# Optimization experiments

Hardware: AMD Instinct MI355X
Metric: run time of the kernel (lower is better)

The kernel has to match this reference:

```python
import jax, jax.numpy as jnp
import numpy as np

D_MODEL = 1024
N_HEADS = 16
DEPTH = D_MODEL // N_HEADS  # 64
BATCH, SEQ = 4, 2048


def setup_inputs() -> dict:
    key = jax.random.key(0)
    ks = jax.random.split(key, 8)
    x = jax.random.normal(ks[0], (BATCH, SEQ, D_MODEL), dtype=jnp.float32)
    # Per-head Dense(depth) weights stacked over heads: [H, d_model, depth]
    s = 1.0 / np.sqrt(D_MODEL)
    Wq = jax.random.normal(ks[1], (N_HEADS, D_MODEL, DEPTH), dtype=jnp.float32) * s
    Wk = jax.random.normal(ks[2], (N_HEADS, D_MODEL, DEPTH), dtype=jnp.float32) * s
    Wv = jax.random.normal(ks[3], (N_HEADS, D_MODEL, DEPTH), dtype=jnp.float32) * s
    bq = jnp.zeros((N_HEADS, DEPTH), dtype=jnp.float32)
    bk = jnp.zeros((N_HEADS, DEPTH), dtype=jnp.float32)
    bv = jnp.zeros((N_HEADS, DEPTH), dtype=jnp.float32)
    Wo = jax.random.normal(ks[4], (D_MODEL, D_MODEL), dtype=jnp.float32) * s
    bo = jnp.zeros((D_MODEL,), dtype=jnp.float32)
    return {"x": x, "Wq": Wq, "bq": bq, "Wk": Wk, "bk": bk,
            "Wv": Wv, "bv": bv, "Wo": Wo, "bo": bo}


def reference(x, Wq, bq, Wk, bk, Wv, bv, Wo, bo):
    # Per-head projections, batched over heads: [b, h, s, depth]
    q = jnp.einsum('bsd,hde->bhse', x, Wq) + bq[None, :, None, :]
    k = jnp.einsum('bsd,hde->bhse', x, Wk) + bk[None, :, None, :]
    v = jnp.einsum('bsd,hde->bhse', x, Wv) + bv[None, :, None, :]
    scale = 1.0 / jnp.sqrt(jnp.float32(DEPTH))
    scores = jnp.einsum('bhqe,bhke->bhqk', q, k) * scale  # [b, h, s, s]
    attn = jax.nn.softmax(scores, axis=-1)
    z = jnp.einsum('bhqk,bhke->bhqe', attn, v)  # [b, h, s, depth]
    # Concat heads along last axis (head-major order matches tf.concat of per-head outputs)
    multi_head = z.transpose(0, 2, 1, 3).reshape(BATCH, SEQ, D_MODEL)
    return multi_head @ Wo + bo
```

## Files before the change

kernel.cpp:

```cpp
#include <hip/hip_runtime.h>

typedef unsigned short u16;
typedef __bf16 bf16x8 __attribute__((ext_vector_type(8)));
typedef float f32x4 __attribute__((ext_vector_type(4)));
typedef float f32x16 __attribute__((ext_vector_type(16)));
typedef unsigned int u32x4 __attribute__((ext_vector_type(4)));
typedef unsigned int u32x2 __attribute__((ext_vector_type(2)));

__device__ __forceinline__ u16 f2b(float f) {
  union { float f; unsigned u; } v; v.f = f;
  return (u16)((v.u + 0x7fffu + ((v.u >> 16) & 1u)) >> 16);
}

__device__ __forceinline__ unsigned pkbf(float a, float b) {
#if __has_builtin(__builtin_amdgcn_cvt_pk_bf16_f32)
  typedef __bf16 bf16x2v __attribute__((ext_vector_type(2)));
  bf16x2v r = __builtin_amdgcn_cvt_pk_bf16_f32(a, b);
  return __builtin_bit_cast(unsigned, r);
#else
  unsigned ua = __builtin_bit_cast(unsigned, a) + 0x8000u;
  unsigned ub = __builtin_bit_cast(unsigned, b) + 0x8000u;
  return __builtin_amdgcn_perm(ub, ua, 0x07060302u);
#endif
}

__device__ __forceinline__ float fexp2(float x) {
#if __has_builtin(__builtin_amdgcn_exp2f)
  return __builtin_amdgcn_exp2f(x);
#else
  return exp2f(x);
#endif
}

__device__ __forceinline__ bf16x8 ldfrag(const u16* p) {
  u32x4 r = *(const u32x4*)p;
  return __builtin_bit_cast(bf16x8, r);
}

#define GLOAD_LDS16(gp, lp)                                                        \
  __builtin_amdgcn_global_load_lds((const __attribute__((address_space(1))) void*)(gp), \
                                   (__attribute__((address_space(3))) void*)(lp), 16, 0, 0)

#define MFMA32(a, b, c) __builtin_amdgcn_mfma_f32_32x32x16_bf16((a), (b), (c), 0, 0, 0)

#define QSC 0.18033688011f


__global__ __launch_bounds__(256) void k_pack(const float* __restrict__ x,
                                              const float* __restrict__ Wq,
                                              const float* __restrict__ Wk,
                                              const float* __restrict__ Wv,
                                              const float* __restrict__ Wo,
                                              u16* __restrict__ xb,
                                              u16* __restrict__ wqkv,
                                              u16* __restrict__ wo_t) {
  const int bid = blockIdx.x, tid = threadIdx.x;
  if (bid < 4096) {
    int i = (bid * 256 + tid) * 8;
    float4 v0 = *(const float4*)(x + i);
    float4 v1 = *(const float4*)(x + i + 4);
    u32x4 o;
    o[0] = pkbf(v0.x, v0.y);
    o[1] = pkbf(v0.z, v0.w);
    o[2] = pkbf(v1.x, v1.y);
    o[3] = pkbf(v1.z, v1.w);
    *(u32x4*)(xb + i) = o;
    return;
  }
  __shared__ u16 tile[64][65];
  if (bid < 4864) {
    int b2 = bid - 4096;
    int p = b2 >> 8, rem = b2 & 255, h = rem >> 4, dt = rem & 15;
    const float* W = (p == 0) ? Wq : (p == 1) ? Wk : Wv;
    for (int i = tid; i < 4096; i += 256) {
      int d = i >> 6, e = i & 63;
      tile[e][d] = f2b(W[h * 65536 + (dt * 64 + d) * 64 + e]);
    }
    __syncthreads();
    for (int i = tid; i < 4096; i += 256) {
      int e = i >> 6, d = i & 63;
      wqkv[(size_t)(p * 1024 + h * 64 + e) * 1024 + dt * 64 + d] = tile[e][d];
    }
  } else {
    int b2 = bid - 4864;
    int kt = b2 >> 4, nt = b2 & 15;
    for (int i = tid; i < 4096; i += 256) {
      int dk = i >> 6, de = i & 63;
      tile[de][dk] = f2b(Wo[(size_t)(kt * 64 + dk) * 1024 + nt * 64 + de]);
    }
    __syncthreads();
    for (int i = tid; i < 4096; i += 256) {
      int de = i >> 6, dk = i & 63;
      wo_t[(size_t)(nt * 64 + de) * 1024 + kt * 64 + dk] = tile[de][dk];
    }
  }
}


template <bool SWAP>
__device__ __forceinline__ void gemm_core32(const u16* __restrict__ A, const u16* __restrict__ Bt,
                                            int row0, int col0, u16* As, u16* Bs, f32x16 acc[2][2]) {
  const int tid = threadIdx.x, w = tid >> 6, lane = tid & 63;
  const int l31 = lane & 31, hi = lane >> 5;
  const int wm = (w >> 1) * 64, wn = (w & 1) * 64;
  for (int k0 = 0; k0 < 1024; k0 += 32) {
#pragma unroll
    for (int i = 0; i < 2; i++) {
      int bse = (w * 2 + i) * 512;
      int flat = bse + lane * 8;
      int r = flat >> 5, c = flat & 31;
      GLOAD_LDS16(A + (size_t)(row0 + r) * 1024 + k0 + c, As + bse);
      GLOAD_LDS16(Bt + (size_t)(col0 + r) * 1024 + k0 + c, Bs + bse);
    }
    __syncthreads();
    bf16x8 af[2][2], bfr[2][2];
#pragma unroll
    for (int t = 0; t < 2; t++)
#pragma unroll
      for (int s = 0; s < 2; s++) {
        af[t][s] = ldfrag(As + (wm + t * 32 + l31) * 32 + s * 16 + hi * 8);
        bfr[t][s] = ldfrag(Bs + (wn + t * 32 + l31) * 32 + s * 16 + hi * 8);
      }
#pragma unroll
    for (int mt = 0; mt < 2; mt++)
#pragma unroll
      for (int nt = 0; nt < 2; nt++)
#pragma unroll
        for (int s = 0; s < 2; s++)
          acc[mt][nt] = SWAP ? MFMA32(bfr[nt][s], af[mt][s], acc[mt][nt])
                             : MFMA32(af[mt][s], bfr[nt][s], acc[mt][nt]);
    __syncthreads();
  }
}


__global__ __launch_bounds__(256) void k_gemm_qkv(const u16* __restrict__ xb, const u16* __restrict__ wt,
                                                  const float* __restrict__ bq, const float* __restrict__ bk,
                                                  const float* __restrict__ bv,
                                                  u16* __restrict__ qo, u16* __restrict__ ko,
                                                  u16* __restrict__ vto) {
  __shared__ u16 As[4096], Bs[4096];
  f32x16 acc[2][2];
#pragma unroll
  for (int a = 0; a < 2; a++)
#pragma unroll
    for (int b = 0; b < 2; b++)
#pragma unroll
      for (int r = 0; r < 16; r++) acc[a][b][r] = 0.f;

  const int row0 = blockIdx.x * 128, col0 = blockIdx.y * 128;
  const int p = blockIdx.y >> 3;
  const int colr = (blockIdx.y & 7) * 128;
  const int tid = threadIdx.x, w = tid >> 6, lane = tid & 63;
  const int l31 = lane & 31, hi = lane >> 5;
  const int wm = (w >> 1) * 64, wn = (w & 1) * 64;

  if (p == 2) {
    gemm_core32<true>(xb, wt, row0, col0, As, Bs, acc);
#pragma unroll
    for (int mt = 0; mt < 2; mt++) {
      int rb = row0 + wm + mt * 32;
      int b_ = rb >> 11;
      int s_ = (rb & 2047) + l31;
#pragma unroll
      for (int nt = 0; nt < 2; nt++) {
        int ebase = colr + wn + nt * 32;
#pragma unroll
        for (int g = 0; g < 4; g++) {
          float4 bvv = *(const float4*)(bv + ebase + g * 8 + hi * 4);
#pragma unroll
          for (int j = 0; j < 4; j++) {
            int rem = ebase + g * 8 + hi * 4 + j;
            int h = rem >> 6, e = rem & 63;
            float val = acc[mt][nt][g * 4 + j] + (&bvv.x)[j];
            vto[(((size_t)(b_ * 16 + h)) * 64 + e) * 2048 + s_] = f2b(val);
          }
        }
      }
    }
  } else {
    gemm_core32<false>(xb, wt, row0, col0, As, Bs, acc);
    u16* dst = (p == 0) ? qo : ko;
    const float* bias = (p == 0) ? bq : bk;
    const float qsc = (p == 0) ? QSC : 1.0f;
#pragma unroll
    for (int nt = 0; nt < 2; nt++) {
      int rem = colr + wn + nt * 32 + l31;
      int h = rem >> 6, e = rem & 63;
      float bval = bias[rem];
#pragma unroll
      for (int mt = 0; mt < 2; mt++) {
        int rb = row0 + wm + mt * 32;
        int b_ = rb >> 11, sb = rb & 2047;
        size_t obase = ((size_t)(b_ * 16 + h) * 2048) * 64 + e;
#pragma unroll
        for (int reg = 0; reg < 16; reg++) {
          int s_ = sb + (reg & 3) + 8 * (reg >> 2) + 4 * hi;
          float val = (acc[mt][nt][reg] + bval) * qsc;
          dst[obase + (size_t)s_ * 64] = f2b(val);
        }
      }
    }
  }
}


__global__ __launch_bounds__(256) void k_gemm_out(const u16* __restrict__ zb, const u16* __restrict__ wt,
                                                  const float* __restrict__ bo, float* __restrict__ out) {
  __shared__ u16 As[4096], Bs[4096];
  f32x16 acc[2][2];
#pragma unroll
  for (int a = 0; a < 2; a++)
#pragma unroll
    for (int b = 0; b < 2; b++)
#pragma unroll
      for (int r = 0; r < 16; r++) acc[a][b][r] = 0.f;

  const int row0 = blockIdx.x * 128, col0 = blockIdx.y * 128;
  gemm_core32<false>(zb, wt, row0, col0, As, Bs, acc);

  const int tid = threadIdx.x, w = tid >> 6, lane = tid & 63;
  const int l31 = lane & 31, hi = lane >> 5;
  const int wm = (w >> 1) * 64, wn = (w & 1) * 64;
#pragma unroll
  for (int nt = 0; nt < 2; nt++) {
    int c = col0 + wn + nt * 32 + l31;
    float bval = bo[c];
#pragma unroll
    for (int mt = 0; mt < 2; mt++) {
      int rb = row0 + wm + mt * 32;
#pragma unroll
      for (int reg = 0; reg < 16; reg++) {
        int r = rb + (reg & 3) + 8 * (reg >> 2) + 4 * hi;
        out[(size_t)r * 1024 + c] = acc[mt][nt][reg] + bval;
      }
    }
  }
}


__global__ __launch_bounds__(256, 2) void k_attn(const u16* __restrict__ q, const u16* __restrict__ k,
                                                 const u16* __restrict__ vt, u16* __restrict__ z) {
  __shared__ u16 Ks[64 * 72], Vs[64 * 72], Ps[4][64 * 72];
  const int tid = threadIdx.x, w = tid >> 6, lane = tid & 63;
  const int l31 = lane & 31, hi = lane >> 5;
  const int bh = blockIdx.y, s0 = blockIdx.x * 256;
  const size_t base = (size_t)bh * 2048 * 64;
  const int qrow0 = s0 + w * 64;

  bf16x8 qf[2][4];
#pragma unroll
  for (int u = 0; u < 2; u++) {
    const u16* qp = q + base + (size_t)(qrow0 + u * 32 + l31) * 64 + hi * 8;
#pragma unroll
    for (int ks = 0; ks < 4; ks++) qf[u][ks] = ldfrag(qp + ks * 16);
  }

  f32x16 accT[2][2];
  f32x16 lvec[2];
#pragma unroll
  for (int u = 0; u < 2; u++) {
#pragma unroll
    for (int r = 0; r < 16; r++) { accT[u][0][r] = 0.f; accT[u][1][r] = 0.f; lvec[u][r] = 0.f; }
  }

  const int srow = tid >> 3;
  const int scol = (tid & 7) * 8;
  const u16* kg = k + base;
  const u16* vg = vt + base;

  u32x4 kr0, kr1, vr0, vr1;
  kr0 = *(const u32x4*)(kg + (size_t)srow * 64 + scol);
  kr1 = *(const u32x4*)(kg + (size_t)(srow + 32) * 64 + scol);
  vr0 = *(const u32x4*)(vg + (size_t)srow * 2048 + scol);
  vr1 = *(const u32x4*)(vg + (size_t)(srow + 32) * 2048 + scol);

  u16* Pw = Ps[w];

  for (int kc = 0; kc < 2048; kc += 64) {
    __syncthreads();
    *(u32x4*)&Ks[srow * 72 + scol] = kr0;
    *(u32x4*)&Ks[(srow + 32) * 72 + scol] = kr1;
    *(u32x4*)&Vs[srow * 72 + scol] = vr0;
    *(u32x4*)&Vs[(srow + 32) * 72 + scol] = vr1;
    __syncthreads();
    if (kc + 64 < 2048) {
      int kn = kc + 64;
      kr0 = *(const u32x4*)(kg + (size_t)(kn + srow) * 64 + scol);
      kr1 = *(const u32x4*)(kg + (size_t)(kn + srow + 32) * 64 + scol);
      vr0 = *(const u32x4*)(vg + (size_t)srow * 2048 + kn + scol);
      vr1 = *(const u32x4*)(vg + (size_t)(srow + 32) * 2048 + kn + scol);
    }

#pragma unroll
    for (int t = 0; t < 2; t++) {
      f32x16 scA, scB;
#pragma unroll
      for (int r = 0; r < 16; r++) { scA[r] = 0.f; scB[r] = 0.f; }
#pragma unroll
      for (int ks = 0; ks < 4; ks++) {
        bf16x8 kf = ldfrag(&Ks[(t * 32 + l31) * 72 + ks * 16 + hi * 8]);
        scA = MFMA32(kf, qf[0][ks], scA);
        scB = MFMA32(kf, qf[1][ks], scB);
      }
#pragma unroll
      for (int r = 0; r < 16; r++) scA[r] = fexp2(scA[r]);
      lvec[0] += scA;
#pragma unroll
      for (int r = 0; r < 16; r++) scB[r] = fexp2(scB[r]);
      lvec[1] += scB;
#pragma unroll
      for (int r4 = 0; r4 < 4; r4++) {
        u32x2 d;
        d[0] = pkbf(scA[r4 * 4 + 0], scA[r4 * 4 + 1]);
        d[1] = pkbf(scA[r4 * 4 + 2], scA[r4 * 4 + 3]);
        *(u32x2*)&Pw[l31 * 72 + t * 32 + r4 * 8 + hi * 4] = d;
        u32x2 e;
        e[0] = pkbf(scB[r4 * 4 + 0], scB[r4 * 4 + 1]);
        e[1] = pkbf(scB[r4 * 4 + 2], scB[r4 * 4 + 3]);
        *(u32x2*)&Pw[(32 + l31) * 72 + t * 32 + r4 * 8 + hi * 4] = e;
      }
    }

#pragma unroll
    for (int ks = 0; ks < 4; ks++) {
      bf16x8 vf0 = ldfrag(&Vs[(0 * 32 + l31) * 72 + ks * 16 + hi * 8]);
      bf16x8 vf1 = ldfrag(&Vs[(1 * 32 + l31) * 72 + ks * 16 + hi * 8]);
      bf16x8 pf0 = ldfrag(&Pw[l31 * 72 + ks * 16 + hi * 8]);
      bf16x8 pf1 = ldfrag(&Pw[(32 + l31) * 72 + ks * 16 + hi * 8]);
      accT[0][0] = MFMA32(vf0, pf0, accT[0][0]);
      accT[0][1] = MFMA32(vf1, pf0, accT[0][1]);
      accT[1][0] = MFMA32(vf0, pf1, accT[1][0]);
      accT[1][1] = MFMA32(vf1, pf1, accT[1][1]);
    }
  }

  const int b_ = bh >> 4, h = bh & 15;
#pragma unroll
  for (int u = 0; u < 2; u++) {
    float l = 0.f;
#pragma unroll
    for (int r = 0; r < 16; r++) l += lvec[u][r];
    l += __shfl_xor(l, 32);
    float inv = 1.f / l;
    int qrow = qrow0 + u * 32 + l31;
    u16* zr = z + ((size_t)(b_ * 2048 + qrow)) * 1024 + h * 64;
#pragma unroll
    for (int et = 0; et < 2; et++)
#pragma unroll
      for (int rr = 0; rr < 16; rr += 2) {
        unsigned pkd = pkbf(accT[u][et][rr] * inv, accT[u][et][rr + 1] * inv);
        int e = et * 32 + (rr & 3) + 8 * (rr >> 2) + 4 * hi;
        *(unsigned*)&zr[e] = pkd;
      }
  }
}


extern "C" void kernel_launch(void* const* d_in, const int* in_sizes, int n_in,
                              void* d_out, int out_size, void* d_ws, size_t ws_size,
                              hipStream_t stream) {
  (void)in_sizes; (void)n_in; (void)out_size;
  const float* x  = (const float*)d_in[0];
  const float* Wq = (const float*)d_in[1];
  const float* bq = (const float*)d_in[2];
  const float* Wk = (const float*)d_in[3];
  const float* bk = (const float*)d_in[4];
  const float* Wv = (const float*)d_in[5];
  const float* bv = (const float*)d_in[6];
  const float* Wo = (const float*)d_in[7];
  const float* bo = (const float*)d_in[8];
  float* out = (float*)d_out;
  char* ws = (char*)d_ws;
  if (ws_size < 92274688u) return;

  u16* xb   = (u16*)(ws + 0);
  u16* wqkv = (u16*)(ws + 16777216);
  u16* wo_t = (u16*)(ws + 23068672);
  u16* qb   = (u16*)(ws + 25165824);
  u16* kb   = (u16*)(ws + 41943040);
  u16* vtb  = (u16*)(ws + 58720256);
  u16* zb   = (u16*)(ws + 75497472);

  k_pack<<<5120, 256, 0, stream>>>(x, Wq, Wk, Wv, Wo, xb, wqkv, wo_t);
  k_gemm_qkv<<<dim3(64, 24), 256, 0, stream>>>(xb, wqkv, bq, bk, bv, qb, kb, vtb);
  k_attn<<<dim3(8, 64), 256, 0, stream>>>(qb, kb, vtb, zb);
  k_gemm_out<<<dim3(64, 8), 256, 0, stream>>>(zb, wo_t, bo, out);
}
```

Before: 299.0 us.

## Keep P in registers via permlane swap and double-buffer K/V in LDS

The attention kernel now builds the P operand for the PV matmul directly in registers, using v_permlane32_swap to rearrange the packed bf16 exp scores. This removes the per-wave LDS round trip through the Ps scratch buffer. K/V tiles are double-buffered in LDS, which leaves one barrier per iteration instead of two. Row sums are reduced to a scalar each step rather than kept as a 16-wide vector, and s_setprio is raised around the MFMA blocks. The changes rely on the permlane layout matching the MFMA B-operand layout, and the in-register P raises register pressure.

```diff
diff --git a/kernel.cpp b/kernel.cpp
--- a/kernel.cpp
+++ b/kernel.cpp
@@ -35,6 +35,37 @@
 __device__ __forceinline__ bf16x8 ldfrag(const u16* p) {
   u32x4 r = *(const u32x4*)p;
   return __builtin_bit_cast(bf16x8, r);
+}
+
+__device__ __forceinline__ void plswap(unsigned& dst, unsigned& src) {
+  asm("v_permlane32_swap_b32 %0, %1" : "+v"(dst), "+v"(src));
+}
+
+__device__ __forceinline__ float sum16(const f32x16& v) {
+  float a = (v[0] + v[1]) + (v[2] + v[3]);
+  float b = (v[4] + v[5]) + (v[6] + v[7]);
+  float c = (v[8] + v[9]) + (v[10] + v[11]);
+  float d = (v[12] + v[13]) + (v[14] + v[15]);
+  return (a + b) + (c + d);
+}
+
+__device__ __forceinline__ void build_frags(const f32x16& sc, bf16x8& fLo, bf16x8& fHi) {
+  unsigned a0 = pkbf(sc[0], sc[1]);
+  unsigned a1 = pkbf(sc[2], sc[3]);
+  unsigned b0 = pkbf(sc[4], sc[5]);
+  unsigned b1 = pkbf(sc[6], sc[7]);
+  plswap(a0, b0);
+  plswap(a1, b1);
+  u32x4 f; f[0] = a0; f[1] = a1; f[2] = b0; f[3] = b1;
+  fLo = __builtin_bit_cast(bf16x8, f);
+  unsigned c0 = pkbf(sc[8], sc[9]);
+  unsigned c1 = pkbf(sc[10], sc[11]);
+  unsigned d0 = pkbf(sc[12], sc[13]);
+  unsigned d1 = pkbf(sc[14], sc[15]);
+  plswap(c0, d0);
+  plswap(c1, d1);
+  u32x4 g; g[0] = c0; g[1] = c1; g[2] = d0; g[3] = d1;
+  fHi = __builtin_bit_cast(bf16x8, g);
 }
 
 #define GLOAD_LDS16(gp, lp)                                                        \
@@ -241,7 +272,7 @@
 
 __global__ __launch_bounds__(256, 2) void k_attn(const u16* __restrict__ q, const u16* __restrict__ k,
                                                  const u16* __restrict__ vt, u16* __restrict__ z) {
-  __shared__ u16 Ks[64 * 72], Vs[64 * 72], Ps[4][64 * 72];
+  __shared__ u16 Ks[2][64 * 72], Vs[2][64 * 72];
   const int tid = threadIdx.x, w = tid >> 6, lane = tid & 63;
   const int l31 = lane & 31, hi = lane >> 5;
   const int bh = blockIdx.y, s0 = blockIdx.x * 256;
@@ -257,90 +288,92 @@
   }
 
   f32x16 accT[2][2];
-  f32x16 lvec[2];
-#pragma unroll
-  for (int u = 0; u < 2; u++) {
-#pragma unroll
-    for (int r = 0; r < 16; r++) { accT[u][0][r] = 0.f; accT[u][1][r] = 0.f; lvec[u][r] = 0.f; }
-  }
+  float ls[2] = {0.f, 0.f};
+#pragma unroll
+  for (int u = 0; u < 2; u++)
+#pragma unroll
+    for (int r = 0; r < 16; r++) { accT[u][0][r] = 0.f; accT[u][1][r] = 0.f; }
 
   const int srow = tid >> 3;
   const int scol = (tid & 7) * 8;
   const u16* kg = k + base;
   const u16* vg = vt + base;
 
-  u32x4 kr0, kr1, vr0, vr1;
-  kr0 = *(const u32x4*)(kg + (size_t)srow * 64 + scol);
-  kr1 = *(const u32x4*)(kg + (size_t)(srow + 32) * 64 + scol);
-  vr0 = *(const u32x4*)(vg + (size_t)srow * 2048 + scol);
-  vr1 = *(const u32x4*)(vg + (size_t)(srow + 32) * 2048 + scol);
-
-  u16* Pw = Ps[w];
+  u32x4 kr0 = *(const u32x4*)(kg + (size_t)srow * 64 + scol);
+  u32x4 kr1 = *(const u32x4*)(kg + (size_t)(srow + 32) * 64 + scol);
+  u32x4 vr0 = *(const u32x4*)(vg + (size_t)srow * 2048 + scol);
+  u32x4 vr1 = *(const u32x4*)(vg + (size_t)(srow + 32) * 2048 + scol);
+  *(u32x4*)&Ks[0][srow * 72 + scol] = kr0;
+  *(u32x4*)&Ks[0][(srow + 32) * 72 + scol] = kr1;
+  *(u32x4*)&Vs[0][srow * 72 + scol] = vr0;
+  *(u32x4*)&Vs[0][(srow + 32) * 72 + scol] = vr1;
+  kr0 = *(const u32x4*)(kg + (size_t)(64 + srow) * 64 + scol);
+  kr1 = *(const u32x4*)(kg + (size_t)(64 + srow + 32) * 64 + scol);
+  vr0 = *(const u32x4*)(vg + (size_t)srow * 2048 + 64 + scol);
+  vr1 = *(const u32x4*)(vg + (size_t)(srow + 32) * 2048 + 64 + scol);
+  __syncthreads();
 
   for (int kc = 0; kc < 2048; kc += 64) {
-    __syncthreads();
-    *(u32x4*)&Ks[srow * 72 + scol] = kr0;
-    *(u32x4*)&Ks[(srow + 32) * 72 + scol] = kr1;
-    *(u32x4*)&Vs[srow * 72 + scol] = vr0;
-    *(u32x4*)&Vs[(srow + 32) * 72 + scol] = vr1;
-    __syncthreads();
-    if (kc + 64 < 2048) {
-      int kn = kc + 64;
-      kr0 = *(const u32x4*)(kg + (size_t)(kn + srow) * 64 + scol);
-      kr1 = *(const u32x4*)(kg + (size_t)(kn + srow + 32) * 64 + scol);
-      vr0 = *(const u32x4*)(vg + (size_t)srow * 2048 + kn + scol);
-      vr1 = *(const u32x4*)(vg + (size_t)(srow + 32) * 2048 + kn + scol);
-    }
-
+    const int buf = (kc >> 6) & 1;
+    const u16* Kb = &Ks[buf][0];
+    const u16* Vb = &Vs[buf][0];
+
+    bf16x8 pf[2][4];
 #pragma unroll
     for (int t = 0; t < 2; t++) {
       f32x16 scA, scB;
 #pragma unroll
       for (int r = 0; r < 16; r++) { scA[r] = 0.f; scB[r] = 0.f; }
+      __builtin_amdgcn_s_setprio(1);
 #pragma unroll
       for (int ks = 0; ks < 4; ks++) {
-        bf16x8 kf = ldfrag(&Ks[(t * 32 + l31) * 72 + ks * 16 + hi * 8]);
+        bf16x8 kf = ldfrag(Kb + (t * 32 + l31) * 72 + ks * 16 + hi * 8);
         scA = MFMA32(kf, qf[0][ks], scA);
         scB = MFMA32(kf, qf[1][ks], scB);
       }
+      __builtin_amdgcn_s_setprio(0);
 #pragma unroll
       for (int r = 0; r < 16; r++) scA[r] = fexp2(scA[r]);
-      lvec[0] += scA;
 #pragma unroll
       for (int r = 0; r < 16; r++) scB[r] = fexp2(scB[r]);
-      lvec[1] += scB;
-#pragma unroll
-      for (int r4 = 0; r4 < 4; r4++) {
-        u32x2 d;
-        d[0] = pkbf(scA[r4 * 4 + 0], scA[r4 * 4 + 1]);
-        d[1] = pkbf(scA[r4 * 4 + 2], scA[r4 * 4 + 3]);
-        *(u32x2*)&Pw[l31 * 72 + t * 32 + r4 * 8 + hi * 4] = d;
-        u32x2 e;
-        e[0] = pkbf(scB[r4 * 4 + 0], scB[r4 * 4 + 1]);
-        e[1] = pkbf(scB[r4 * 4 + 2], scB[r4 * 4 + 3]);
-        *(u32x2*)&Pw[(32 + l31) * 72 + t * 32 + r4 * 8 + hi * 4] = e;
-      }
-    }
-
+      ls[0] += sum16(scA);
+      ls[1] += sum16(scB);
+      build_frags(scA, pf[0][2 * t], pf[0][2 * t + 1]);
+      build_frags(scB, pf[1][2 * t], pf[1][2 * t + 1]);
+    }
+
+    if (kc + 64 < 2048) {
+      *(u32x4*)&Ks[buf ^ 1][srow * 72 + scol] = kr0;
+      *(u32x4*)&Ks[buf ^ 1][(srow + 32) * 72 + scol] = kr1;
+      *(u32x4*)&Vs[buf ^ 1][srow * 72 + scol] = vr0;
+      *(u32x4*)&Vs[buf ^ 1][(srow + 32) * 72 + scol] = vr1;
+      if (kc + 128 < 2048) {
+        int kn = kc + 128;
+        kr0 = *(const u32x4*)(kg + (size_t)(kn + srow) * 64 + scol);
+        kr1 = *(const u32x4*)(kg + (size_t)(kn + srow + 32) * 64 + scol);
+        vr0 = *(const u32x4*)(vg + (size_t)srow * 2048 + kn + scol);
+        vr1 = *(const u32x4*)(vg + (size_t)(srow + 32) * 2048 + kn + scol);
+      }
+    }
+
+    __builtin_amdgcn_s_setprio(1);
 #pragma unroll
     for (int ks = 0; ks < 4; ks++) {
-      bf16x8 vf0 = ldfrag(&Vs[(0 * 32 + l31) * 72 + ks * 16 + hi * 8]);
-      bf16x8 vf1 = ldfrag(&Vs[(1 * 32 + l31) * 72 + ks * 16 + hi * 8]);
-      bf16x8 pf0 = ldfrag(&Pw[l31 * 72 + ks * 16 + hi * 8]);
-      bf16x8 pf1 = ldfrag(&Pw[(32 + l31) * 72 + ks * 16 + hi * 8]);
-      accT[0][0] = MFMA32(vf0, pf0, accT[0][0]);
-      accT[0][1] = MFMA32(vf1, pf0, accT[0][1]);
-      accT[1][0] = MFMA32(vf0, pf1, accT[1][0]);
-      accT[1][1] = MFMA32(vf1, pf1, accT[1][1]);
-    }
+      bf16x8 vf0 = ldfrag(Vb + (0 * 32 + l31) * 72 + ks * 16 + hi * 8);
+      bf16x8 vf1 = ldfrag(Vb + (1 * 32 + l31) * 72 + ks * 16 + hi * 8);
+      accT[0][0] = MFMA32(vf0, pf[0][ks], accT[0][0]);
+      accT[0][1] = MFMA32(vf1, pf[0][ks], accT[0][1]);
+      accT[1][0] = MFMA32(vf0, pf[1][ks], accT[1][0]);
+      accT[1][1] = MFMA32(vf1, pf[1][ks], accT[1][1]);
+    }
+    __builtin_amdgcn_s_setprio(0);
+    __syncthreads();
   }
 
   const int b_ = bh >> 4, h = bh & 15;
 #pragma unroll
   for (int u = 0; u < 2; u++) {
-    float l = 0.f;
-#pragma unroll
-    for (int r = 0; r < 16; r++) l += lvec[u][r];
+    float l = ls[u];
     l += __shfl_xor(l, 32);
     float inv = 1.f / l;
     int qrow = qrow0 + u * 32 + l31;
```

Result: faster. 290.3 us (-2.9%).
